# Kernel optimization log

Hardware: AMD Instinct MI355X
Metric: run time of the kernel (lower is better)

The kernel has to match this reference:

```python
import jax, jax.numpy as jnp
import numpy as np

TOTAL_WORDS = 10000
EMBED_LEN = 100
SEQ_LEN = 80
UNITS = 128
BATCH = 4096


def setup_inputs() -> dict:
    key = jax.random.key(0)
    ks = jax.random.split(key, 8)
    s = 0.05  # small init scale to keep gates unsaturated
    return {
        "tokens": jax.random.randint(ks[0], (BATCH, SEQ_LEN), 0, TOTAL_WORDS),
        "emb": jax.random.normal(ks[1], (TOTAL_WORDS, EMBED_LEN), jnp.float32) * s,
        "W1": jax.random.normal(ks[2], (EMBED_LEN, 4 * UNITS), jnp.float32) * s,
        "U1": jax.random.normal(ks[3], (UNITS, 4 * UNITS), jnp.float32) * s,
        "b1": jnp.zeros((4 * UNITS,), jnp.float32),
        "W2": jax.random.normal(ks[4], (UNITS, 4 * UNITS), jnp.float32) * s,
        "U2": jax.random.normal(ks[5], (UNITS, 4 * UNITS), jnp.float32) * s,
        "b2": jnp.zeros((4 * UNITS,), jnp.float32),
        "Wd": jax.random.normal(ks[6], (UNITS, 1), jnp.float32) * s,
        "bd": jnp.zeros((1,), jnp.float32),
    }


def _lstm(x_seq, W, U, b, return_sequences):
    # x_seq: [B, T, D]; Keras gate order: i, f, g(c), o
    B = x_seq.shape[0]
    H = U.shape[0]

    def step(carry, x_t):
        h, c = carry
        z = x_t @ W + h @ U + b  # [B, 4H]
        i, f, g, o = jnp.split(z, 4, axis=-1)
        c = jax.nn.sigmoid(f) * c + jax.nn.sigmoid(i) * jnp.tanh(g)
        h = jax.nn.sigmoid(o) * jnp.tanh(c)
        return (h, c), h

    h0 = jnp.zeros((B, H), x_seq.dtype)
    (hT, _), hs = jax.lax.scan(step, (h0, h0), jnp.swapaxes(x_seq, 0, 1))
    return jnp.swapaxes(hs, 0, 1) if return_sequences else hT


def reference(tokens, emb, W1, U1, b1, W2, U2, b2, Wd, bd):
    x = emb[tokens]                      # [B, T, E]
    h1 = _lstm(x, W1, U1, b1, True)      # [B, T, H]
    h2 = _lstm(h1, W2, U2, b2, False)    # [B, H] (last step)
    return jax.nn.sigmoid(h2 @ Wd + bd)  # [B, 1]
```

## Files before the change

kernel.cpp:

```cpp
#include <hip/hip_runtime.h>
#include <hip/hip_bf16.h>

#define T_SEQ 80
#define EMB   100
#define HU    128
#define G4    512
#define BR    16
#define THR   512
#define LOG2E 1.44269504f

typedef __attribute__((ext_vector_type(8))) short bfrag;
typedef __attribute__((ext_vector_type(4))) float f32x4;

#define OFF_EW1P 0ull
#define OFF_U1T  10240000ull
#define OFF_U2T  (OFF_U1T + 131072ull)
#define OFF_W2T  (OFF_U2T + 131072ull)

__device__ inline unsigned short f2bf(float x) {
    __hip_bfloat16 h = __float2bfloat16(x);
    unsigned short u; __builtin_memcpy(&u, &h, 2); return u;
}
__device__ inline float bf2f(unsigned short u) {
    unsigned int v = ((unsigned int)u) << 16;
    float f; __builtin_memcpy(&f, &v, 4); return f;
}
__device__ inline float sig_p(float zp) {
    return __builtin_amdgcn_rcpf(1.f + __builtin_amdgcn_exp2f(zp));
}
__device__ inline float tanh_p(float zp) {
    return 1.f - 2.f * __builtin_amdgcn_rcpf(1.f + __builtin_amdgcn_exp2f(zp));
}
__device__ inline float tanh_r(float x) {
    return 1.f - 2.f * __builtin_amdgcn_rcpf(1.f + __builtin_amdgcn_exp2f(2.f * LOG2E * x));
}
__device__ inline float sig_r(float x) {
    return __builtin_amdgcn_rcpf(1.f + __builtin_amdgcn_exp2f(-LOG2E * x));
}
__device__ inline bfrag ld_frag(const unsigned short* buf, int row, int kk, int lhi) {
    int byte = (row * 256 + kk * 64 + lhi * 16) ^ ((row & 7) << 4);
    return *(const bfrag*)((const char*)buf + byte);
}
__device__ inline void st_h(unsigned short* buf, int rr, int u, unsigned short v) {
    int byte = ((rr * 256 + u * 2) ^ ((rr & 7) << 4));
    *(unsigned short*)((char*)buf + byte) = v;
}
__device__ inline void barrier_lgkm() {
    asm volatile("s_waitcnt lgkmcnt(0)\n\ts_barrier" ::: "memory");
}

#define K2_TOKS 8
#define VOCAB_BLKS 1250
__global__ __launch_bounds__(512) void prep_all(
    const float* __restrict__ emb, const float* __restrict__ W1, const float* __restrict__ b1,
    const float* __restrict__ U1, const float* __restrict__ U2, const float* __restrict__ W2,
    unsigned short* __restrict__ EW1p, unsigned short* __restrict__ U1T,
    unsigned short* __restrict__ U2T, unsigned short* __restrict__ W2T) {
    const int tid = threadIdx.x;
    if (blockIdx.x < VOCAB_BLKS) {
        __shared__ float embs[K2_TOKS * EMB];
        const int tok0 = blockIdx.x * K2_TOKS;
        for (int i = tid; i < K2_TOKS * EMB; i += 512) embs[i] = emb[tok0 * EMB + i];
        __syncthreads();
        const int c = tid;
        const int g = c >> 7, u = c & 127;
        const float scale = (g == 2) ? 2.f * LOG2E : -LOG2E;
        float s[K2_TOKS];
        const float bias = b1[c];
#pragma unroll
        for (int tt = 0; tt < K2_TOKS; tt++) s[tt] = bias;
        for (int e = 0; e < EMB; e++) {
            float wv = W1[e * G4 + c];
#pragma unroll
            for (int tt = 0; tt < K2_TOKS; tt++) s[tt] += embs[tt * EMB + e] * wv;
        }
#pragma unroll
        for (int tt = 0; tt < K2_TOKS; tt++)
            EW1p[(size_t)(tok0 + tt) * G4 + u * 4 + g] = f2bf(s[tt] * scale);
    } else {
#pragma unroll
        for (int r = 0; r < 2; r++) {
            int idx = (blockIdx.x - VOCAB_BLKS) * 1024 + r * 512 + tid;
            int n = idx >> 7, k = idx & 127;
            const float scale = ((n >> 7) == 2) ? 2.f * LOG2E : -LOG2E;
            U1T[n * 128 + k] = f2bf(U1[k * 512 + n] * scale);
            U2T[n * 128 + k] = f2bf(U2[k * 512 + n] * scale);
            W2T[n * 128 + k] = f2bf(W2[k * 512 + n] * scale);
        }
    }
}

__global__ __launch_bounds__(THR, 2) void lstm_fused(
    const int* __restrict__ tokens, const unsigned short* __restrict__ EW1p,
    const unsigned short* __restrict__ U1T, const unsigned short* __restrict__ U2T,
    const unsigned short* __restrict__ W2T, const float* __restrict__ b2,
    const float* __restrict__ Wd, const float* __restrict__ bd, float* __restrict__ out) {

    __shared__ unsigned short w2lds[G4 * HU];
    __shared__ unsigned short h1b[2][BR * HU];
    __shared__ unsigned short h2b[2][BR * HU];
    __shared__ int toklds[BR * T_SEQ];

    const int tid = threadIdx.x;
    const int w   = tid >> 6;
    const int l   = tid & 63;
    const int llo = l & 15, lhi = l >> 4;
    const int u   = w * 16 + llo;
    const int r0  = blockIdx.x * BR;

    {
        for (int i = tid; i < G4 * HU / 8; i += THR) {
            int n = i >> 4, c16 = i & 15;
            int byte = (n * 256 + c16 * 16) ^ ((n & 7) << 4);
            *(uint4*)((char*)w2lds + byte) = *(const uint4*)(W2T + n * 128 + c16 * 8);
        }
    }
    for (int i = tid; i < BR * T_SEQ; i += THR) toklds[i] = tokens[r0 * T_SEQ + i];
    for (int i = tid; i < BR * HU; i += THR) { h2b[0][i] = 0; h2b[1][i] = 0; }

    bfrag u1r[4][4], u2r[4][4];
#pragma unroll
    for (int g = 0; g < 4; g++)
#pragma unroll
        for (int kk = 0; kk < 4; kk++) {
            size_t off = (size_t)(g * 128 + u) * 128 + kk * 32 + lhi * 8;
            u1r[g][kk] = *(const bfrag*)(U1T + off);
            u2r[g][kk] = *(const bfrag*)(U2T + off);
        }
    float bb[4];
#pragma unroll
    for (int g = 0; g < 4; g++) bb[g] = b2[g * 128 + u] * ((g == 2) ? 2.f * LOG2E : -LOG2E);

    float c1[4] = {0, 0, 0, 0}, c2[4] = {0, 0, 0, 0};
    ushort4 zv[4];

    __syncthreads();

#pragma unroll
    for (int j = 0; j < 4; j++) {
        int tok = toklds[(lhi * 4 + j) * T_SEQ + 0];
        zv[j] = *(const ushort4*)(EW1p + (size_t)tok * G4 + u * 4);
    }
#pragma unroll
    for (int j = 0; j < 4; j++) {
        float si = sig_p(bf2f(zv[j].x)), sf = sig_p(bf2f(zv[j].y));
        float tg = tanh_p(bf2f(zv[j].z)), so = sig_p(bf2f(zv[j].w));
        float cn = sf * c1[j] + si * tg;
        c1[j] = cn;
        st_h(h1b[0], lhi * 4 + j, u, f2bf(so * tanh_r(cn)));
    }
#pragma unroll
    for (int j = 0; j < 4; j++) {
        int tok = toklds[(lhi * 4 + j) * T_SEQ + 1];
        zv[j] = *(const ushort4*)(EW1p + (size_t)tok * G4 + u * 4);
    }
    __syncthreads();

    auto phase = [&](int sn, const unsigned short* h1p, const unsigned short* h2p,
                     unsigned short* h1n, unsigned short* h2n) {
        bfrag a1[4], a2[4];
#pragma unroll
        for (int kk = 0; kk < 4; kk++) a1[kk] = ld_frag(h1p, llo, kk, lhi);
#pragma unroll
        for (int kk = 0; kk < 4; kk++) a2[kk] = ld_frag(h2p, llo, kk, lhi);
        f32x4 acc1[4];
#pragma unroll
        for (int j = 0; j < 4; j++) {
            acc1[0][j] = bf2f(zv[j].x); acc1[1][j] = bf2f(zv[j].y);
            acc1[2][j] = bf2f(zv[j].z); acc1[3][j] = bf2f(zv[j].w);
        }
#pragma unroll
        for (int j = 0; j < 4; j++) {
            int tok = toklds[(lhi * 4 + j) * T_SEQ + sn];
            zv[j] = *(const ushort4*)(EW1p + (size_t)tok * G4 + u * 4);
        }
#pragma unroll
        for (int g = 0; g < 4; g++)
#pragma unroll
            for (int kk = 0; kk < 4; kk++)
                acc1[g] = __builtin_amdgcn_mfma_f32_16x16x32_bf16(a1[kk], u1r[g][kk], acc1[g], 0, 0, 0);
        f32x4 acc2[4];
#pragma unroll
        for (int g = 0; g < 4; g++) acc2[g] = (f32x4){bb[g], bb[g], bb[g], bb[g]};
#pragma unroll
        for (int kk = 0; kk < 4; kk++)
#pragma unroll
            for (int g = 0; g < 4; g++)
                acc2[g] = __builtin_amdgcn_mfma_f32_16x16x32_bf16(a2[kk], u2r[g][kk], acc2[g], 0, 0, 0);
        bfrag wfc[4];
#pragma unroll
        for (int kk = 0; kk < 4; kk++) wfc[kk] = ld_frag(w2lds, 0 * 128 + u, kk, lhi);
#pragma unroll
        for (int j = 0; j < 4; j++) {
            float si = sig_p(acc1[0][j]), sf = sig_p(acc1[1][j]);
            float tg = tanh_p(acc1[2][j]), so = sig_p(acc1[3][j]);
            float cn = sf * c1[j] + si * tg;
            c1[j] = cn;
            st_h(h1n, lhi * 4 + j, u, f2bf(so * tanh_r(cn)));
        }
#pragma unroll
        for (int g = 0; g < 4; g++) {
            bfrag wfn[4];
            if (g < 3) {
#pragma unroll
                for (int kk = 0; kk < 4; kk++) wfn[kk] = ld_frag(w2lds, (g + 1) * 128 + u, kk, lhi);
            }
#pragma unroll
            for (int kk = 0; kk < 4; kk++)
                acc2[g] = __builtin_amdgcn_mfma_f32_16x16x32_bf16(a1[kk], wfc[kk], acc2[g], 0, 0, 0);
            if (g < 3) {
#pragma unroll
                for (int kk = 0; kk < 4; kk++) wfc[kk] = wfn[kk];
            }
        }
#pragma unroll
        for (int j = 0; j < 4; j++) {
            float si = sig_p(acc2[0][j]), sf = sig_p(acc2[1][j]);
            float tg = tanh_p(acc2[2][j]), so = sig_p(acc2[3][j]);
            float cn = sf * c2[j] + si * tg;
            c2[j] = cn;
            st_h(h2n, lhi * 4 + j, u, f2bf(so * tanh_r(cn)));
        }
        barrier_lgkm();
    };

    phase(2, h1b[0], h2b[1], h1b[1], h2b[0]);
#pragma unroll 1
    for (int s = 2; s < T_SEQ - 1; s += 2) {
        phase(s + 1, h1b[1], h2b[0], h1b[0], h2b[1]);
        phase((s + 2 < T_SEQ) ? s + 2 : T_SEQ - 1,
              h1b[0], h2b[1], h1b[1], h2b[0]);
    }

    {
        f32x4 acc2[4];
#pragma unroll
        for (int g = 0; g < 4; g++) acc2[g] = (f32x4){bb[g], bb[g], bb[g], bb[g]};
#pragma unroll
        for (int kk = 0; kk < 4; kk++) {
            bfrag a1 = ld_frag(h1b[1], llo, kk, lhi);
#pragma unroll
            for (int g = 0; g < 4; g++) {
                bfrag wf = ld_frag(w2lds, g * 128 + u, kk, lhi);
                acc2[g] = __builtin_amdgcn_mfma_f32_16x16x32_bf16(a1, wf, acc2[g], 0, 0, 0);
            }
        }
#pragma unroll
        for (int kk = 0; kk < 4; kk++) {
            bfrag a2 = ld_frag(h2b[0], llo, kk, lhi);
#pragma unroll
            for (int g = 0; g < 4; g++)
                acc2[g] = __builtin_amdgcn_mfma_f32_16x16x32_bf16(a2, u2r[g][kk], acc2[g], 0, 0, 0);
        }
#pragma unroll
        for (int j = 0; j < 4; j++) {
            float si = sig_p(acc2[0][j]), sf = sig_p(acc2[1][j]);
            float tg = tanh_p(acc2[2][j]), so = sig_p(acc2[3][j]);
            float cn = sf * c2[j] + si * tg;
            c2[j] = cn;
            st_h(h2b[1], lhi * 4 + j, u, f2bf(so * tanh_r(cn)));
        }
    }
    __syncthreads();

    if (w == 0) {
        int r = l >> 2, q = l & 3;
        float s = 0.f;
        for (int k = q * 32; k < q * 32 + 32; k++) {
            int byte = (r * 256 + k * 2) ^ ((r & 7) << 4);
            s += bf2f(*(const unsigned short*)((const char*)h2b[1] + byte)) * Wd[k];
        }
        s += __shfl_xor(s, 1, 64);
        s += __shfl_xor(s, 2, 64);
        if (q == 0) out[r0 + r] = sig_r(s + bd[0]);
    }
}

extern "C" void kernel_launch(void* const* d_in, const int* in_sizes, int n_in,
                              void* d_out, int out_size, void* d_ws, size_t ws_size,
                              hipStream_t stream) {
    const int*   tokens = (const int*)  d_in[0];
    const float* emb    = (const float*)d_in[1];
    const float* W1     = (const float*)d_in[2];
    const float* U1     = (const float*)d_in[3];
    const float* b1     = (const float*)d_in[4];
    const float* W2     = (const float*)d_in[5];
    const float* U2     = (const float*)d_in[6];
    const float* b2     = (const float*)d_in[7];
    const float* Wd     = (const float*)d_in[8];
    const float* bd     = (const float*)d_in[9];
    float* out = (float*)d_out;

    char* ws = (char*)d_ws;
    unsigned short* EW1p = (unsigned short*)(ws + OFF_EW1P);
    unsigned short* U1T  = (unsigned short*)(ws + OFF_U1T);
    unsigned short* U2T  = (unsigned short*)(ws + OFF_U2T);
    unsigned short* W2T  = (unsigned short*)(ws + OFF_W2T);

    prep_all<<<VOCAB_BLKS + 64, 512, 0, stream>>>(emb, W1, b1, U1, U2, W2, EW1p, U1T, U2T, W2T);
    lstm_fused<<<256, THR, 0, stream>>>(tokens, EW1p, U1T, U2T, W2T, b2, Wd, bd, out);
}
```

Measured before the change: 267.3 us.

## Transpose MFMA operands so each lane owns four units, pack h stores, retile prep

Swaps the MFMA A/B operands so the accumulator layout gives each lane four consecutive hidden units for one batch row. That lets h results be packed with v_cvt_pk_bf16 into a single 8-byte LDS store, and the precomputed input projection be fetched with two 16-byte loads instead of four scattered 8-byte loads. The token table is padded to reduce LDS bank conflicts. The embedding-projection prep kernel now handles 64 tokens per block with transposed LDS staging. This changes register pressure and LDS access patterns; the prep kernel now holds 64 accumulators per thread.

```diff
diff --git a/kernel.cpp b/kernel.cpp
--- a/kernel.cpp
+++ b/kernel.cpp
@@ -2,6 +2,7 @@
 #include <hip/hip_bf16.h>
 
 #define T_SEQ 80
+#define TPAD  81
 #define EMB   100
 #define HU    128
 #define G4    512
@@ -21,9 +22,16 @@
     __hip_bfloat16 h = __float2bfloat16(x);
     unsigned short u; __builtin_memcpy(&u, &h, 2); return u;
 }
-__device__ inline float bf2f(unsigned short u) {
-    unsigned int v = ((unsigned int)u) << 16;
-    float f; __builtin_memcpy(&f, &v, 4); return f;
+__device__ inline float lo_bf(unsigned int d) {
+    unsigned int v = d << 16; float f; __builtin_memcpy(&f, &v, 4); return f;
+}
+__device__ inline float hi_bf(unsigned int d) {
+    unsigned int v = d & 0xffff0000u; float f; __builtin_memcpy(&f, &v, 4); return f;
+}
+__device__ inline unsigned int cvt_pk_bf16(float a, float b) {
+    unsigned int d;
+    asm("v_cvt_pk_bf16_f32 %0, %1, %2" : "=v"(d) : "v"(a), "v"(b));
+    return d;
 }
 __device__ inline float sig_p(float zp) {
     return __builtin_amdgcn_rcpf(1.f + __builtin_amdgcn_exp2f(zp));
@@ -41,46 +49,59 @@
     int byte = (row * 256 + kk * 64 + lhi * 16) ^ ((row & 7) << 4);
     return *(const bfrag*)((const char*)buf + byte);
 }
-__device__ inline void st_h(unsigned short* buf, int rr, int u, unsigned short v) {
-    int byte = ((rr * 256 + u * 2) ^ ((rr & 7) << 4));
-    *(unsigned short*)((char*)buf + byte) = v;
-}
 __device__ inline void barrier_lgkm() {
     asm volatile("s_waitcnt lgkmcnt(0)\n\ts_barrier" ::: "memory");
 }
 
-#define K2_TOKS 8
-#define VOCAB_BLKS 1250
+#define PTOK 64
+#define VBLK 157
 __global__ __launch_bounds__(512) void prep_all(
     const float* __restrict__ emb, const float* __restrict__ W1, const float* __restrict__ b1,
     const float* __restrict__ U1, const float* __restrict__ U2, const float* __restrict__ W2,
     unsigned short* __restrict__ EW1p, unsigned short* __restrict__ U1T,
     unsigned short* __restrict__ U2T, unsigned short* __restrict__ W2T) {
     const int tid = threadIdx.x;
-    if (blockIdx.x < VOCAB_BLKS) {
-        __shared__ float embs[K2_TOKS * EMB];
-        const int tok0 = blockIdx.x * K2_TOKS;
-        for (int i = tid; i < K2_TOKS * EMB; i += 512) embs[i] = emb[tok0 * EMB + i];
+    if (blockIdx.x < VBLK) {
+        __shared__ float embs_t[EMB][PTOK + 4];
+        const int tok0 = blockIdx.x * PTOK;
+        for (int i = tid; i < PTOK * EMB; i += 512) {
+            int tt = i / EMB, e = i - tt * EMB;
+            int gi = tok0 * EMB + i;
+            embs_t[e][tt] = (gi < 10000 * EMB) ? emb[gi] : 0.f;
+        }
         __syncthreads();
         const int c = tid;
-        const int g = c >> 7, u = c & 127;
-        const float scale = (g == 2) ? 2.f * LOG2E : -LOG2E;
-        float s[K2_TOKS];
+        const int pos = (c & 127) * 4 + (c >> 7);
+        const float scale = ((c >> 7) == 2) ? 2.f * LOG2E : -LOG2E;
         const float bias = b1[c];
-#pragma unroll
-        for (int tt = 0; tt < K2_TOKS; tt++) s[tt] = bias;
-        for (int e = 0; e < EMB; e++) {
-            float wv = W1[e * G4 + c];
-#pragma unroll
-            for (int tt = 0; tt < K2_TOKS; tt++) s[tt] += embs[tt * EMB + e] * wv;
-        }
-#pragma unroll
-        for (int tt = 0; tt < K2_TOKS; tt++)
-            EW1p[(size_t)(tok0 + tt) * G4 + u * 4 + g] = f2bf(s[tt] * scale);
+        float s[PTOK];
+#pragma unroll
+        for (int tt = 0; tt < PTOK; tt++) s[tt] = bias;
+        for (int e4 = 0; e4 < EMB / 4; e4++) {
+            float w4[4];
+#pragma unroll
+            for (int i = 0; i < 4; i++) w4[i] = W1[(e4 * 4 + i) * G4 + c];
+#pragma unroll
+            for (int i = 0; i < 4; i++) {
+#pragma unroll
+                for (int q = 0; q < PTOK / 4; q++) {
+                    float4 ev = *(const float4*)&embs_t[e4 * 4 + i][q * 4];
+                    s[q * 4 + 0] += ev.x * w4[i];
+                    s[q * 4 + 1] += ev.y * w4[i];
+                    s[q * 4 + 2] += ev.z * w4[i];
+                    s[q * 4 + 3] += ev.w * w4[i];
+                }
+            }
+        }
+#pragma unroll 4
+        for (int tt = 0; tt < PTOK; tt++) {
+            if (tok0 + tt < 10000)
+                EW1p[(size_t)(tok0 + tt) * G4 + pos] = f2bf(s[tt] * scale);
+        }
     } else {
 #pragma unroll
         for (int r = 0; r < 2; r++) {
-            int idx = (blockIdx.x - VOCAB_BLKS) * 1024 + r * 512 + tid;
+            int idx = (blockIdx.x - VBLK) * 1024 + r * 512 + tid;
             int n = idx >> 7, k = idx & 127;
             const float scale = ((n >> 7) == 2) ? 2.f * LOG2E : -LOG2E;
             U1T[n * 128 + k] = f2bf(U1[k * 512 + n] * scale);
@@ -96,10 +117,10 @@
     const unsigned short* __restrict__ W2T, const float* __restrict__ b2,
     const float* __restrict__ Wd, const float* __restrict__ bd, float* __restrict__ out) {
 
-    __shared__ unsigned short w2lds[G4 * HU];
     __shared__ unsigned short h1b[2][BR * HU];
     __shared__ unsigned short h2b[2][BR * HU];
-    __shared__ int toklds[BR * T_SEQ];
+    __shared__ int toklds[BR * TPAD];
+    __shared__ unsigned short w2lds[G4 * HU];
 
     const int tid = threadIdx.x;
     const int w   = tid >> 6;
@@ -107,6 +128,8 @@
     const int llo = l & 15, lhi = l >> 4;
     const int u   = w * 16 + llo;
     const int r0  = blockIdx.x * BR;
+    const int uw  = w * 16 + lhi * 4;
+    const int wb  = (llo * 256 + uw * 2) ^ ((llo & 7) << 4);
 
     {
         for (int i = tid; i < G4 * HU / 8; i += THR) {
@@ -115,7 +138,10 @@
             *(uint4*)((char*)w2lds + byte) = *(const uint4*)(W2T + n * 128 + c16 * 8);
         }
     }
-    for (int i = tid; i < BR * T_SEQ; i += THR) toklds[i] = tokens[r0 * T_SEQ + i];
+    for (int i = tid; i < BR * T_SEQ; i += THR) {
+        int r = i / T_SEQ, t = i - r * T_SEQ;
+        toklds[r * TPAD + t] = tokens[r0 * T_SEQ + i];
+    }
     for (int i = tid; i < BR * HU; i += THR) { h2b[0][i] = 0; h2b[1][i] = 0; }
 
     bfrag u1r[4][4], u2r[4][4];
@@ -132,53 +158,59 @@
     for (int g = 0; g < 4; g++) bb[g] = b2[g * 128 + u] * ((g == 2) ? 2.f * LOG2E : -LOG2E);
 
     float c1[4] = {0, 0, 0, 0}, c2[4] = {0, 0, 0, 0};
-    ushort4 zv[4];
+    uint4 zq0, zq1;
 
     __syncthreads();
 
-#pragma unroll
-    for (int j = 0; j < 4; j++) {
-        int tok = toklds[(lhi * 4 + j) * T_SEQ + 0];
-        zv[j] = *(const ushort4*)(EW1p + (size_t)tok * G4 + u * 4);
-    }
-#pragma unroll
-    for (int j = 0; j < 4; j++) {
-        float si = sig_p(bf2f(zv[j].x)), sf = sig_p(bf2f(zv[j].y));
-        float tg = tanh_p(bf2f(zv[j].z)), so = sig_p(bf2f(zv[j].w));
-        float cn = sf * c1[j] + si * tg;
-        c1[j] = cn;
-        st_h(h1b[0], lhi * 4 + j, u, f2bf(so * tanh_r(cn)));
-    }
-#pragma unroll
-    for (int j = 0; j < 4; j++) {
-        int tok = toklds[(lhi * 4 + j) * T_SEQ + 1];
-        zv[j] = *(const ushort4*)(EW1p + (size_t)tok * G4 + u * 4);
+    {
+        int tok = toklds[llo * TPAD + 0];
+        const char* p = (const char*)(EW1p + (size_t)tok * G4 + w * 64 + lhi * 16);
+        zq0 = *(const uint4*)p; zq1 = *(const uint4*)(p + 16);
+        float hh[4];
+#pragma unroll
+        for (int j = 0; j < 4; j++) {
+            int d0 = j * 2;
+            unsigned int da = (j < 2) ? ((unsigned int*)&zq0)[d0 & 3] : ((unsigned int*)&zq1)[d0 & 3];
+            unsigned int db = (j < 2) ? ((unsigned int*)&zq0)[(d0 + 1) & 3] : ((unsigned int*)&zq1)[(d0 + 1) & 3];
+            float si = sig_p(lo_bf(da)), sf = sig_p(hi_bf(da));
+            float tg = tanh_p(lo_bf(db)), so = sig_p(hi_bf(db));
+            float cn = sf * c1[j] + si * tg;
+            c1[j] = cn;
+            hh[j] = so * tanh_r(cn);
+        }
+        uint2 dv = {cvt_pk_bf16(hh[0], hh[1]), cvt_pk_bf16(hh[2], hh[3])};
+        *(uint2*)((char*)h1b[0] + wb) = dv;
+        tok = toklds[llo * TPAD + 1];
+        p = (const char*)(EW1p + (size_t)tok * G4 + w * 64 + lhi * 16);
+        zq0 = *(const uint4*)p; zq1 = *(const uint4*)(p + 16);
     }
     __syncthreads();
 
     auto phase = [&](int sn, const unsigned short* h1p, const unsigned short* h2p,
                      unsigned short* h1n, unsigned short* h2n) {
-        bfrag a1[4], a2[4];
-#pragma unroll
-        for (int kk = 0; kk < 4; kk++) a1[kk] = ld_frag(h1p, llo, kk, lhi);
-#pragma unroll
-        for (int kk = 0; kk < 4; kk++) a2[kk] = ld_frag(h2p, llo, kk, lhi);
+        bfrag b1f[4], b2f[4];
+#pragma unroll
+        for (int kk = 0; kk < 4; kk++) b1f[kk] = ld_frag(h1p, llo, kk, lhi);
+#pragma unroll
+        for (int kk = 0; kk < 4; kk++) b2f[kk] = ld_frag(h2p, llo, kk, lhi);
         f32x4 acc1[4];
 #pragma unroll
         for (int j = 0; j < 4; j++) {
-            acc1[0][j] = bf2f(zv[j].x); acc1[1][j] = bf2f(zv[j].y);
-            acc1[2][j] = bf2f(zv[j].z); acc1[3][j] = bf2f(zv[j].w);
-        }
-#pragma unroll
-        for (int j = 0; j < 4; j++) {
-            int tok = toklds[(lhi * 4 + j) * T_SEQ + sn];
-            zv[j] = *(const ushort4*)(EW1p + (size_t)tok * G4 + u * 4);
+            unsigned int da = (j < 2) ? ((unsigned int*)&zq0)[(j * 2) & 3] : ((unsigned int*)&zq1)[(j * 2) & 3];
+            unsigned int db = (j < 2) ? ((unsigned int*)&zq0)[(j * 2 + 1) & 3] : ((unsigned int*)&zq1)[(j * 2 + 1) & 3];
+            acc1[0][j] = lo_bf(da); acc1[1][j] = hi_bf(da);
+            acc1[2][j] = lo_bf(db); acc1[3][j] = hi_bf(db);
+        }
+        {
+            int tok = toklds[llo * TPAD + sn];
+            const char* p = (const char*)(EW1p + (size_t)tok * G4 + w * 64 + lhi * 16);
+            zq0 = *(const uint4*)p; zq1 = *(const uint4*)(p + 16);
         }
 #pragma unroll
         for (int g = 0; g < 4; g++)
 #pragma unroll
             for (int kk = 0; kk < 4; kk++)
-                acc1[g] = __builtin_amdgcn_mfma_f32_16x16x32_bf16(a1[kk], u1r[g][kk], acc1[g], 0, 0, 0);
+                acc1[g] = __builtin_amdgcn_mfma_f32_16x16x32_bf16(u1r[g][kk], b1f[kk], acc1[g], 0, 0, 0);
         f32x4 acc2[4];
 #pragma unroll
         for (int g = 0; g < 4; g++) acc2[g] = (f32x4){bb[g], bb[g], bb[g], bb[g]};
@@ -186,40 +218,41 @@
         for (int kk = 0; kk < 4; kk++)
 #pragma unroll
             for (int g = 0; g < 4; g++)
-                acc2[g] = __builtin_amdgcn_mfma_f32_16x16x32_bf16(a2[kk], u2r[g][kk], acc2[g], 0, 0, 0);
-        bfrag wfc[4];
-#pragma unroll
-        for (int kk = 0; kk < 4; kk++) wfc[kk] = ld_frag(w2lds, 0 * 128 + u, kk, lhi);
-#pragma unroll
-        for (int j = 0; j < 4; j++) {
-            float si = sig_p(acc1[0][j]), sf = sig_p(acc1[1][j]);
-            float tg = tanh_p(acc1[2][j]), so = sig_p(acc1[3][j]);
-            float cn = sf * c1[j] + si * tg;
-            c1[j] = cn;
-            st_h(h1n, lhi * 4 + j, u, f2bf(so * tanh_r(cn)));
+                acc2[g] = __builtin_amdgcn_mfma_f32_16x16x32_bf16(u2r[g][kk], b2f[kk], acc2[g], 0, 0, 0);
+        {
+            float hh[4];
+#pragma unroll
+            for (int j = 0; j < 4; j++) {
+                float si = sig_p(acc1[0][j]), sf = sig_p(acc1[1][j]);
+                float tg = tanh_p(acc1[2][j]), so = sig_p(acc1[3][j]);
+                float cn = sf * c1[j] + si * tg;
+                c1[j] = cn;
+                hh[j] = so * tanh_r(cn);
+            }
+            uint2 dv = {cvt_pk_bf16(hh[0], hh[1]), cvt_pk_bf16(hh[2], hh[3])};
+            *(uint2*)((char*)h1n + wb) = dv;
         }
 #pragma unroll
         for (int g = 0; g < 4; g++) {
-            bfrag wfn[4];
-            if (g < 3) {
-#pragma unroll
-                for (int kk = 0; kk < 4; kk++) wfn[kk] = ld_frag(w2lds, (g + 1) * 128 + u, kk, lhi);
+            bfrag wf[4];
+#pragma unroll
+            for (int kk = 0; kk < 4; kk++) wf[kk] = ld_frag(w2lds, g * 128 + u, kk, lhi);
+#pragma unroll
+            for (int kk = 0; kk < 4; kk++)
+                acc2[g] = __builtin_amdgcn_mfma_f32_16x16x32_bf16(wf[kk], b1f[kk], acc2[g], 0, 0, 0);
+        }
+        {
+            float hh[4];
+#pragma unroll
+            for (int j = 0; j < 4; j++) {
+                float si = sig_p(acc2[0][j]), sf = sig_p(acc2[1][j]);
+                float tg = tanh_p(acc2[2][j]), so = sig_p(acc2[3][j]);
+                float cn = sf * c2[j] + si * tg;
+                c2[j] = cn;
+                hh[j] = so * tanh_r(cn);
             }
-#pragma unroll
-            for (int kk = 0; kk < 4; kk++)
-                acc2[g] = __builtin_amdgcn_mfma_f32_16x16x32_bf16(a1[kk], wfc[kk], acc2[g], 0, 0, 0);
-            if (g < 3) {
-#pragma unroll
-                for (int kk = 0; kk < 4; kk++) wfc[kk] = wfn[kk];
-            }
-        }
-#pragma unroll
-        for (int j = 0; j < 4; j++) {
-            float si = sig_p(acc2[0][j]), sf = sig_p(acc2[1][j]);
-            float tg = tanh_p(acc2[2][j]), so = sig_p(acc2[3][j]);
-            float cn = sf * c2[j] + si * tg;
-            c2[j] = cn;
-            st_h(h2n, lhi * 4 + j, u, f2bf(so * tanh_r(cn)));
+            uint2 dv = {cvt_pk_bf16(hh[0], hh[1]), cvt_pk_bf16(hh[2], hh[3])};
+            *(uint2*)((char*)h2n + wb) = dv;
         }
         barrier_lgkm();
     };
@@ -233,33 +266,39 @@
     }
 
     {
+        bfrag b1f[4], b2f[4];
+#pragma unroll
+        for (int kk = 0; kk < 4; kk++) b1f[kk] = ld_frag(h1b[1], llo, kk, lhi);
+#pragma unroll
+        for (int kk = 0; kk < 4; kk++) b2f[kk] = ld_frag(h2b[0], llo, kk, lhi);
         f32x4 acc2[4];
 #pragma unroll
         for (int g = 0; g < 4; g++) acc2[g] = (f32x4){bb[g], bb[g], bb[g], bb[g]};
 #pragma unroll
-        for (int kk = 0; kk < 4; kk++) {
-            bfrag a1 = ld_frag(h1b[1], llo, kk, lhi);
-#pragma unroll
-            for (int g = 0; g < 4; g++) {
-                bfrag wf = ld_frag(w2lds, g * 128 + u, kk, lhi);
-                acc2[g] = __builtin_amdgcn_mfma_f32_16x16x32_bf16(a1, wf, acc2[g], 0, 0, 0);
-            }
-        }
-#pragma unroll
-        for (int kk = 0; kk < 4; kk++) {
-            bfrag a2 = ld_frag(h2b[0], llo, kk, lhi);
+        for (int kk = 0; kk < 4; kk++)
 #pragma unroll
             for (int g = 0; g < 4; g++)
-                acc2[g] = __builtin_amdgcn_mfma_f32_16x16x32_bf16(a2, u2r[g][kk], acc2[g], 0, 0, 0);
-        }
+                acc2[g] = __builtin_amdgcn_mfma_f32_16x16x32_bf16(u2r[g][kk], b2f[kk], acc2[g], 0, 0, 0);
+#pragma unroll
+        for (int g = 0; g < 4; g++) {
+            bfrag wf[4];
+#pragma unroll
+            for (int kk = 0; kk < 4; kk++) wf[kk] = ld_frag(w2lds, g * 128 + u, kk, lhi);
+#pragma unroll
+            for (int kk = 0; kk < 4; kk++)
+                acc2[g] = __builtin_amdgcn_mfma_f32_16x16x32_bf16(wf[kk], b1f[kk], acc2[g], 0, 0, 0);
+        }
+        float hh[4];
 #pragma unroll
         for (int j = 0; j < 4; j++) {
             float si = sig_p(acc2[0][j]), sf = sig_p(acc2[1][j]);
             float tg = tanh_p(acc2[2][j]), so = sig_p(acc2[3][j]);
             float cn = sf * c2[j] + si * tg;
             c2[j] = cn;
-            st_h(h2b[1], lhi * 4 + j, u, f2bf(so * tanh_r(cn)));
-        }
+            hh[j] = so * tanh_r(cn);
+        }
+        uint2 dv = {cvt_pk_bf16(hh[0], hh[1]), cvt_pk_bf16(hh[2], hh[3])};
+        *(uint2*)((char*)h2b[1] + wb) = dv;
     }
     __syncthreads();
 
@@ -268,7 +307,7 @@
         float s = 0.f;
         for (int k = q * 32; k < q * 32 + 32; k++) {
             int byte = (r * 256 + k * 2) ^ ((r & 7) << 4);
-            s += bf2f(*(const unsigned short*)((const char*)h2b[1] + byte)) * Wd[k];
+            s += lo_bf(*(const unsigned short*)((const char*)h2b[1] + byte)) * Wd[k];
         }
         s += __shfl_xor(s, 1, 64);
         s += __shfl_xor(s, 2, 64);
@@ -297,6 +336,6 @@
     unsigned short* U2T  = (unsigned short*)(ws + OFF_U2T);
     unsigned short* W2T  = (unsigned short*)(ws + OFF_W2T);
 
-    prep_all<<<VOCAB_BLKS + 64, 512, 0, stream>>>(emb, W1, b1, U1, U2, W2, EW1p, U1T, U2T, W2T);
+    prep_all<<<VBLK + 64, 512, 0, stream>>>(emb, W1, b1, U1, U2, W2, EW1p, U1T, U2T, W2T);
     lstm_fused<<<256, THR, 0, stream>>>(tokens, EW1p, U1T, U2T, W2T, b2, Wd, bd, out);
 }
```

Result: slower. 290.4 us (+8.6%).
